# Kernel tuning notes

Hardware: AMD Instinct MI355X
Metric: run time of the kernel (lower is better)

The kernel has to match this reference:

```python
import jax, jax.numpy as jnp
import numpy as np

CHUNK = 64      # chunk_size
DIM = 128       # dim; memory state is a DIM x DIM fast-weight matrix (flattened)
BASE_LR = 0.005 # base inner-loop step size
META_LR = 0.01  # step size for the per-parameter learning-rate (optimizer) state


def setup_inputs():
    key = jax.random.key(0)
    k1, k2 = jax.random.split(key)
    B, L, D = 16, 8192, DIM
    X = jax.random.normal(k1, (B, L, D), jnp.float32)
    # init memory: small random D x D matrix, flattened (like LFLTM.init_params())
    init_mem = jax.random.normal(k2, (D * D,), jnp.float32) * 0.09
    # init optimizer state: per-parameter lr logits (sigmoid(0)=0.5)
    init_opt = jnp.zeros((D * D,), jnp.float32)
    return {"X": X, "init_mem": init_mem, "init_opt": init_opt}


def _forward(X, init_mem, init_opt):
    B, L, D = X.shape
    pad = (-L) % CHUNK
    Xp = jnp.pad(X, ((0, 0), (0, pad), (0, 0)))
    nC = Xp.shape[1] // CHUNK
    # [nC, B, CHUNK, D] so lax.scan iterates over chunks (the python loop in torch)
    Xc = Xp.reshape(B, nC, CHUNK, D).transpose(1, 0, 2, 3)

    def chunk_step(carry, x):
        mem, opt = carry                      # [B, D*D] each
        W = mem.reshape(B, D, D)
        # per-token gradient of 0.5*||W k - v||^2 with k = v = x, taken at the
        # chunk-start memory state (matches vmap(..., (0,0,None,None)) in torch)
        err = jnp.einsum('bij,bcj->bci', W, x) - x          # [B, C, D]
        g = jnp.einsum('bci,bcj->bcij', err, x).reshape(B, CHUNK, D * D)
        lr = jax.nn.sigmoid(opt)[:, None, :]                # [B, 1, D*D]
        mem_upd = BASE_LR * lr * g                          # memory update per token
        opt_upd = META_LR * (g * g) * lr * (1.0 - lr)       # lr-logit update per token
        cmu = jnp.cumsum(mem_upd, axis=1)                   # [B, C, D*D]
        cou = jnp.cumsum(opt_upd, axis=1)
        # memory path: state after each token's update (mem - cumsum)
        mem_path = (mem[:, None, :] - cmu).reshape(B, CHUNK, D, D)
        # retrieval: out_t = M_t @ q_t with q_t = x_t
        out = jnp.einsum('bcij,bcj->bci', mem_path, x)      # [B, C, D]
        new_carry = (mem - cmu[:, -1], opt - cou[:, -1])
        return new_carry, out

    mem0 = jnp.broadcast_to(init_mem, (B, D * D))
    opt0 = jnp.broadcast_to(init_opt, (B, D * D))
    _, outs = jax.lax.scan(chunk_step, (mem0, opt0), Xc)    # outs: [nC, B, C, D]
    outs = outs.transpose(1, 0, 2, 3).reshape(B, nC * CHUNK, D)
    return outs[:, :L]


def reference(X, init_mem, init_opt):
    return _forward(X, init_mem, init_opt)
```

## Files before the change

### kernel.cpp

```cpp
#include <hip/hip_runtime.h>
#include <math.h>

#define D 128
#define CHK 64
#define NCHUNK 128
#define LSEQ 8192
#define B_LR 0.005f
#define M_LR 0.01f

typedef float f2 __attribute__((ext_vector_type(2)));

__device__ __forceinline__ f2 pk_mul(f2 a, f2 b){ f2 d; asm("v_pk_mul_f32 %0, %1, %2" : "=v"(d) : "v"(a), "v"(b)); return d; }
__device__ __forceinline__ void pk_fma_acc(f2 &acc, f2 a, f2 b){ asm("v_pk_fma_f32 %0, %1, %2, %0" : "+v"(acc) : "v"(a), "v"(b)); }

template<int C>
__device__ __forceinline__ float dppx(float x){
  return __int_as_float(__builtin_amdgcn_update_dpp(0, __float_as_int(x), C, 0xF, 0xF, true));
}
__device__ __forceinline__ void pl32swap(float &a, float &b){ asm("v_permlane32_swap_b32 %0, %1" : "+v"(a), "+v"(b)); }
__device__ __forceinline__ void pl16swap(float &a, float &b){ asm("v_permlane16_swap_b32 %0, %1" : "+v"(a), "+v"(b)); }

__device__ __forceinline__ float butterfly64(float* a, int lane){
  #pragma unroll
  for (int t = 0; t < 32; ++t){ pl32swap(a[t], a[t+32]); a[t] = a[t] + a[t+32]; }
  #pragma unroll
  for (int t = 0; t < 16; ++t){ pl16swap(a[t], a[t+16]); a[t] = a[t] + a[t+16]; }
  const bool h8 = (lane & 8) != 0, h4 = (lane & 4) != 0, h2 = (lane & 2) != 0, h1 = (lane & 1) != 0;
  #pragma unroll
  for (int t = 0; t < 8; ++t){
    float send = h8 ? a[t] : a[t+8];
    float keep = h8 ? a[t+8] : a[t];
    a[t] = keep + dppx<0x128>(send);
  }
  #pragma unroll
  for (int t = 0; t < 4; ++t){
    float send = h4 ? a[t] : a[t+4];
    float keep = h4 ? a[t+4] : a[t];
    a[t] = keep + __int_as_float(__builtin_amdgcn_ds_swizzle(__float_as_int(send), 0x101F));
  }
  #pragma unroll
  for (int t = 0; t < 2; ++t){
    float send = h2 ? a[t] : a[t+2];
    float keep = h2 ? a[t+2] : a[t];
    a[t] = keep + dppx<0x4E>(send);
  }
  float send = h1 ? a[0] : a[1];
  float keep = h1 ? a[1] : a[0];
  return keep + dppx<0xB1>(send);
}

__device__ __forceinline__ void gl_lds16(const float* g, float* l){
  __builtin_amdgcn_global_load_lds((const __attribute__((address_space(1))) float*)g,
                                   (__attribute__((address_space(3))) float*)l, 16, 0, 0);
}

__global__ __launch_bounds__(256, 2) void lfltm_fwd(
    const float* __restrict__ X,
    const float* __restrict__ init_mem,
    const float* __restrict__ init_opt,
    float* __restrict__ out)
{
  __shared__ float xs[2][CHK * D];
  __shared__ float es[4][CHK];
  __shared__ float outs[2][CHK * 5];

  const int tid  = threadIdx.x;
  const int w    = tid >> 6;
  const int lane = tid & 63;

  const int bid  = blockIdx.x;
  const int xcd  = bid & 7;
  const int b    = xcd + 8 * ((bid >> 3) & 1);
  const int rg   = bid >> 4;
  const int i    = rg * 4 + w;

  const float* __restrict__ Xb = X + (size_t)b * (LSEQ * D);
  float* __restrict__ Ob       = out + (size_t)b * (LSEQ * D);

  f2 m, o;
  m.x = init_mem[i * D + 2*lane];
  m.y = init_mem[i * D + 2*lane + 1];
  o.x = init_opt[i * D + 2*lane];
  o.y = init_opt[i * D + 2*lane + 1];
  f2 u;
  u.x = (2*lane     == i) ? 1.0f : 0.0f;
  u.y = (2*lane + 1 == i) ? 1.0f : 0.0f;

  #pragma unroll
  for (int r = 0; r < 8; ++r)
    gl_lds16(Xb + (r*256 + tid)*4, &xs[0][(r*256 + tid)*4]);
  __syncthreads();

  for (int ch = 0; ch < NCHUNK; ++ch) {
    const int cur = ch & 1;

    if (ch > 0) {
      const int c = tid >> 2, rr = tid & 3;
      Ob[(size_t)((ch-1)*CHK + c)*D + rg*4 + rr] = outs[cur ^ 1][c*5 + rr];
    }

    {
      int chn = ch + 1; if (chn >= NCHUNK) chn = NCHUNK - 1;
      const float* gb = Xb + (size_t)chn * (CHK * D);
      #pragma unroll
      for (int r = 0; r < 8; ++r)
        gl_lds16(gb + (r*256 + tid)*4, &xs[cur ^ 1][(r*256 + tid)*4]);
    }

    const float xci = Xb[(size_t)(ch*CHK + lane)*D + i];

    f2 lr;
    lr.x = 1.0f / (1.0f + __expf(-o.x));
    lr.y = 1.0f / (1.0f + __expf(-o.y));
    const f2 mp = m - u;

    const float* xb = &xs[cur][2*lane];

    float arr[CHK];
    #pragma unroll
    for (int c = 0; c < CHK; ++c){
      f2 x2 = *(const f2*)(xb + c*D);
      f2 t  = pk_mul(mp, x2);
      arr[c] = t.x + t.y;
    }
    const float e_own = butterfly64(arr, lane);
    es[w][lane] = e_own;

    f2 S; S.x = 0.f; S.y = 0.f;
    f2 Q; Q.x = 0.f; Q.y = 0.f;
    #pragma unroll
    for (int cg = 0; cg < CHK/4; ++cg){
      float4 e4 = *(const float4*)&es[w][cg*4];
      #pragma unroll
      for (int uu = 0; uu < 4; ++uu){
        const int c = cg*4 + uu;
        const float ec = (uu==0)?e4.x:(uu==1)?e4.y:(uu==2)?e4.z:e4.w;
        f2 e2; e2.x = ec; e2.y = ec;
        f2 x2 = *(const f2*)(xb + c*D);
        f2 ex = pk_mul(e2, x2);
        pk_fma_acc(S, lr, ex);
        f2 pt = pk_mul(x2, S);
        pk_fma_acc(Q, ex, ex);
        arr[c] = pt.x + pt.y;
      }
    }
    const float p = butterfly64(arr, lane);

    outs[cur][lane*5 + w] = e_own + xci - B_LR * p;

    m = m - B_LR * S;
    f2 g = lr - lr * lr;
    o = o - M_LR * (g * Q);

    __syncthreads();
  }

  {
    const int c = tid >> 2, rr = tid & 3;
    Ob[(size_t)((NCHUNK-1)*CHK + c)*D + rg*4 + rr] = outs[(NCHUNK-1)&1][c*5 + rr];
  }
}

extern "C" void kernel_launch(void* const* d_in, const int* in_sizes, int n_in,
                              void* d_out, int out_size, void* d_ws, size_t ws_size,
                              hipStream_t stream) {
    const float* X  = (const float*)d_in[0];
    const float* im = (const float*)d_in[1];
    const float* io = (const float*)d_in[2];
    float* O        = (float*)d_out;
    hipLaunchKernelGGL(lfltm_fwd, dim3(512), dim3(256), 0, stream, X, im, io, O);
}
```

Measured before the change: 719.9 us.

## Split each memory row across two waves with 512-thread blocks

Each row of the fast-weight matrix is now handled by two wavefronts, each owning 64 columns with one float per lane, where before a single wave held two columns per lane in packed-math registers. Block size doubles to 512 threads. Partial row sums from the two halves are combined through LDS, which adds two extra block-wide barriers per chunk. The aim is more waves in flight and shorter per-lane serial work per chunk, at the cost of packed FMA use and extra synchronisation.

```diff
diff --git a/kernel.cpp b/kernel.cpp
--- a/kernel.cpp
+++ b/kernel.cpp
@@ -8,11 +8,6 @@
 #define B_LR 0.005f
 #define M_LR 0.01f
 
-typedef float f2 __attribute__((ext_vector_type(2)));
-
-__device__ __forceinline__ f2 pk_mul(f2 a, f2 b){ f2 d; asm("v_pk_mul_f32 %0, %1, %2" : "=v"(d) : "v"(a), "v"(b)); return d; }
-__device__ __forceinline__ void pk_fma_acc(f2 &acc, f2 a, f2 b){ asm("v_pk_fma_f32 %0, %1, %2, %0" : "+v"(acc) : "v"(a), "v"(b)); }
-
 template<int C>
 __device__ __forceinline__ float dppx(float x){
   return __int_as_float(__builtin_amdgcn_update_dpp(0, __float_as_int(x), C, 0xF, 0xF, true));
@@ -22,9 +17,9 @@
 
 __device__ __forceinline__ float butterfly64(float* a, int lane){
   #pragma unroll
-  for (int t = 0; t < 32; ++t){ pl32swap(a[t], a[t+32]); a[t] = a[t] + a[t+32]; }
+  for (int t = 0; t < 32; ++t){ float u=a[t], w=a[t+32]; pl32swap(u,w); a[t]=u+w; }
   #pragma unroll
-  for (int t = 0; t < 16; ++t){ pl16swap(a[t], a[t+16]); a[t] = a[t] + a[t+16]; }
+  for (int t = 0; t < 16; ++t){ float u=a[t], w=a[t+16]; pl16swap(u,w); a[t]=u+w; }
   const bool h8 = (lane & 8) != 0, h4 = (lane & 4) != 0, h2 = (lane & 2) != 0, h1 = (lane & 1) != 0;
   #pragma unroll
   for (int t = 0; t < 8; ++t){
@@ -54,47 +49,47 @@
                                    (__attribute__((address_space(3))) float*)l, 16, 0, 0);
 }
 
-__global__ __launch_bounds__(256, 2) void lfltm_fwd(
+__global__ __launch_bounds__(512, 4) void lfltm_fwd(
     const float* __restrict__ X,
     const float* __restrict__ init_mem,
     const float* __restrict__ init_opt,
     float* __restrict__ out)
 {
   __shared__ float xs[2][CHK * D];
-  __shared__ float es[4][CHK];
+  __shared__ float ebuf[8][CHK];
+  __shared__ float esb[8][CHK];
+  __shared__ float pbuf[8][CHK];
   __shared__ float outs[2][CHK * 5];
 
   const int tid  = threadIdx.x;
   const int w    = tid >> 6;
   const int lane = tid & 63;
+  const int r    = w >> 1;
+  const int h    = w & 1;
 
-  const int bid  = blockIdx.x;
-  const int xcd  = bid & 7;
-  const int b    = xcd + 8 * ((bid >> 3) & 1);
-  const int rg   = bid >> 4;
-  const int i    = rg * 4 + w;
+  const int bid = blockIdx.x;
+  const int xcd = bid & 7;
+  const int b   = xcd + 8 * ((bid >> 3) & 1);
+  const int rg  = bid >> 4;
+  const int i   = rg * 4 + r;
+  const int jl  = h * 64 + lane;
 
   const float* __restrict__ Xb = X + (size_t)b * (LSEQ * D);
   float* __restrict__ Ob       = out + (size_t)b * (LSEQ * D);
 
-  f2 m, o;
-  m.x = init_mem[i * D + 2*lane];
-  m.y = init_mem[i * D + 2*lane + 1];
-  o.x = init_opt[i * D + 2*lane];
-  o.y = init_opt[i * D + 2*lane + 1];
-  f2 u;
-  u.x = (2*lane     == i) ? 1.0f : 0.0f;
-  u.y = (2*lane + 1 == i) ? 1.0f : 0.0f;
+  float m = init_mem[i * D + jl];
+  float o = init_opt[i * D + jl];
+  const float u = (jl == i) ? 1.0f : 0.0f;
 
   #pragma unroll
-  for (int r = 0; r < 8; ++r)
-    gl_lds16(Xb + (r*256 + tid)*4, &xs[0][(r*256 + tid)*4]);
+  for (int k = 0; k < 4; ++k)
+    gl_lds16(Xb + (k*512 + tid)*4, &xs[0][(k*512 + tid)*4]);
   __syncthreads();
 
   for (int ch = 0; ch < NCHUNK; ++ch) {
     const int cur = ch & 1;
 
-    if (ch > 0) {
+    if (ch > 0 && tid < 256) {
       const int c = tid >> 2, rr = tid & 3;
       Ob[(size_t)((ch-1)*CHK + c)*D + rg*4 + rr] = outs[cur ^ 1][c*5 + rr];
     }
@@ -103,61 +98,61 @@
       int chn = ch + 1; if (chn >= NCHUNK) chn = NCHUNK - 1;
       const float* gb = Xb + (size_t)chn * (CHK * D);
       #pragma unroll
-      for (int r = 0; r < 8; ++r)
-        gl_lds16(gb + (r*256 + tid)*4, &xs[cur ^ 1][(r*256 + tid)*4]);
+      for (int k = 0; k < 4; ++k)
+        gl_lds16(gb + (k*512 + tid)*4, &xs[cur ^ 1][(k*512 + tid)*4]);
     }
 
     const float xci = Xb[(size_t)(ch*CHK + lane)*D + i];
 
-    f2 lr;
-    lr.x = 1.0f / (1.0f + __expf(-o.x));
-    lr.y = 1.0f / (1.0f + __expf(-o.y));
-    const f2 mp = m - u;
+    const float lr = 1.0f / (1.0f + __expf(-o));
+    const float mp = m - u;
 
-    const float* xb = &xs[cur][2*lane];
+    const float* xcol = &xs[cur][jl];
 
     float arr[CHK];
     #pragma unroll
-    for (int c = 0; c < CHK; ++c){
-      f2 x2 = *(const f2*)(xb + c*D);
-      f2 t  = pk_mul(mp, x2);
-      arr[c] = t.x + t.y;
-    }
-    const float e_own = butterfly64(arr, lane);
-    es[w][lane] = e_own;
+    for (int c = 0; c < CHK; ++c)
+      arr[c] = mp * xcol[c*D];
+    const float epart = butterfly64(arr, lane);
 
-    f2 S; S.x = 0.f; S.y = 0.f;
-    f2 Q; Q.x = 0.f; Q.y = 0.f;
+    ebuf[w][lane] = epart;
+    __syncthreads();
+    const float efull = epart + ebuf[w ^ 1][lane];
+    esb[w][lane] = efull;
+
+    float S = 0.f, Q = 0.f;
     #pragma unroll
     for (int cg = 0; cg < CHK/4; ++cg){
-      float4 e4 = *(const float4*)&es[w][cg*4];
+      float4 e4 = *(const float4*)&esb[w][cg*4];
       #pragma unroll
       for (int uu = 0; uu < 4; ++uu){
         const int c = cg*4 + uu;
         const float ec = (uu==0)?e4.x:(uu==1)?e4.y:(uu==2)?e4.z:e4.w;
-        f2 e2; e2.x = ec; e2.y = ec;
-        f2 x2 = *(const f2*)(xb + c*D);
-        f2 ex = pk_mul(e2, x2);
-        pk_fma_acc(S, lr, ex);
-        f2 pt = pk_mul(x2, S);
-        pk_fma_acc(Q, ex, ex);
-        arr[c] = pt.x + pt.y;
+        const float x  = xcol[c*D];
+        const float ex = ec * x;
+        S = fmaf(lr, ex, S);
+        arr[c] = x * S;
+        Q = fmaf(ex, ex, Q);
       }
     }
-    const float p = butterfly64(arr, lane);
+    const float ppart = butterfly64(arr, lane);
 
-    outs[cur][lane*5 + w] = e_own + xci - B_LR * p;
+    pbuf[w][lane] = ppart;
+    __syncthreads();
+    if (h == 0) {
+      const float p = ppart + pbuf[w ^ 1][lane];
+      outs[cur][lane*5 + r] = efull + xci - B_LR * p;
+    }
 
-    m = m - B_LR * S;
-    f2 g = lr - lr * lr;
-    o = o - M_LR * (g * Q);
+    m = fmaf(-B_LR, S, m);
+    o = fmaf(-M_LR * lr * (1.f - lr), Q, o);
 
     __syncthreads();
   }
 
-  {
+  if (tid < 256) {
     const int c = tid >> 2, rr = tid & 3;
-    Ob[(size_t)((NCHUNK-1)*CHK + c)*D + rg*4 + rr] = outs[(NCHUNK-1)&1][c*5 + rr];
+    Ob[(size_t)((NCHUNK-1)*CHK + c)*D + rg*4 + rr] = outs[(NCHUNK-1) & 1][c*5 + rr];
   }
 }
 
@@ -168,5 +163,5 @@
     const float* im = (const float*)d_in[1];
     const float* io = (const float*)d_in[2];
     float* O        = (float*)d_out;
-    hipLaunchKernelGGL(lfltm_fwd, dim3(512), dim3(256), 0, stream, X, im, io, O);
+    hipLaunchKernelGGL(lfltm_fwd, dim3(512), dim3(512), 0, stream, X, im, io, O);
 }
```

Measured after the change: 677.7 us. 5.9% less time.
